# Optimization experiments

Measured on AMD Instinct MI355X. Metric: run time of the kernel, lower is better.

## Reference

```python
import jax, jax.numpy as jnp
import numpy as np

N_IN = 4096      # input features
N_NPB = 64       # neurons (inputs) per branch column
N_B = 64         # branches
N_NEXT_H = 256   # next hidden width
COLS = N_B * N_NEXT_H
BATCH = 128


def setup_inputs() -> dict:
    key = jax.random.key(0)
    k1, k2, k3 = jax.random.split(key, 3)
    x = jax.random.normal(k1, (BATCH, N_IN), dtype=jnp.float32)
    # torch kaiming_normal_ on (n_npb, cols): fan_in = cols, gain = sqrt(2)
    std = np.sqrt(2.0 / COLS).astype(np.float32)
    w = jax.random.normal(k2, (N_NPB, COLS), dtype=jnp.float32) * std
    # random per-column input indices (the module's all_branch_indices)
    idx = jax.random.randint(k3, (N_NPB, COLS), 0, N_IN, dtype=jnp.int32)
    return {"x": x, "w": w, "idx": idx}


def _last_write_mask(idx):
    # (row, col) targets. keep[k, c] is True iff no k' > k has idx[k', c] == idx[k, c].
    eq = idx[:, None, :] == idx[None, :, :]                    # [K, K, C]
    later = jnp.triu(jnp.ones((N_NPB, N_NPB), bool), 1)        # k' > k
    return ~jnp.any(eq & later[:, :, None], axis=1)            # [K, C]


def reference(x, w, idx):
    keep = _last_write_mask(idx)
    w_eff = jnp.where(keep, w, jnp.zeros((), x.dtype))         # [K, C]
    cols = jnp.broadcast_to(jnp.arange(COLS), (N_NPB, COLS))
    # scatter weights into dense [n_in, cols] (equals torch's clone+index_put)
    dense = jnp.zeros((N_IN, COLS), x.dtype).at[idx, cols].add(w_eff)
    out = x @ dense                                            # [B, COLS]
    return out.reshape(-1, N_B, N_NEXT_H)
```

## Files before the change

kernel.cpp:

```cpp
#include <hip/hip_runtime.h>

#define N_IN   4096
#define N_NPB  64
#define COLS   16384
#define BATCH  128

typedef unsigned int       uint;
typedef unsigned short     ushort;
typedef unsigned long long u64;
typedef __attribute__((ext_vector_type(2))) _Float16 h2;


template <int KBASE>
static __device__ __forceinline__ uint compute_bits(const int* __restrict__ ip) {
  int v[64 - KBASE];
#pragma unroll
  for (int k = 0; k < 64 - KBASE; ++k) v[k] = ip[(KBASE + k) * COLS];
  uint bits = 0;
#pragma unroll
  for (int j = 0; j < 16; ++j) {
    uint m = 0xffffffffu;
#pragma unroll
    for (int kp = j + 1; kp < 64 - KBASE; ++kp)
      m = min(m, (uint)(v[j] ^ v[kp]));
    bits |= (m != 0u) ? (1u << j) : 0u;
  }
  return bits;
}

__global__ __launch_bounds__(256, 4) void prep_kernel(
    const float* __restrict__ x, const int* __restrict__ idx,
    ushort* __restrict__ xTh, ushort* __restrict__ keep16) {
  const int bid = blockIdx.x;
  const int tid = threadIdx.x;
  if (bid < 512) {
    __shared__ float tile[32][33];
    const int i0 = (bid & 127) * 32;
    const int b0 = (bid >> 7) * 32;
    const int tx = tid & 31;
    const int ty = tid >> 5;
#pragma unroll
    for (int j = 0; j < 32; j += 8)
      tile[ty + j][tx] = x[(b0 + ty + j) * N_IN + i0 + tx];
    __syncthreads();
#pragma unroll
    for (int j = 0; j < 32; j += 8)
      xTh[(i0 + ty + j) * BATCH + b0 + tx] =
          __builtin_bit_cast(ushort, (_Float16)tile[tx][ty + j]);
  } else {
    const int kg = __builtin_amdgcn_readfirstlane(tid >> 6);
    const int c  = (bid - 512) * 64 + (tid & 63);
    const int* ip = idx + c;
    uint bits;
    if      (kg == 0) bits = compute_bits<0>(ip);
    else if (kg == 1) bits = compute_bits<16>(ip);
    else if (kg == 2) bits = compute_bits<32>(ip);
    else              bits = compute_bits<48>(ip);
    keep16[c * 4 + kg] = (ushort)bits;
  }
}

__global__ __launch_bounds__(512, 8) void branch_main_kernel(
    const float* __restrict__ w, const int* __restrict__ idx,
    const u64* __restrict__ keep, const ushort* __restrict__ xTh,
    float* __restrict__ out) {
  __shared__ u64   pk[N_NPB][16];
  __shared__ float res[2][16][132];

  const int tid = threadIdx.x;
  const int c0  = blockIdx.x * 16;

  {
    const int cl = tid & 15;
    const int k0 = (tid >> 4) * 2;
    const u64 km = keep[c0 + cl];
#pragma unroll
    for (int p = 0; p < 2; ++p) {
      const int k   = k0 + p;
      const int row = idx[k * COLS + c0 + cl];
      float wv      = w[k * COLS + c0 + cl];
      wv = ((km >> k) & 1ull) ? wv : 0.0f;
      const uint hb = (uint)__builtin_bit_cast(ushort, (_Float16)wv);
      pk[k][cl] = ((u64)((hb << 16) | hb) << 32) | ((u64)((uint)row << 8));
    }
  }
  __syncthreads();

  const int wave  = tid >> 6;
  const int khalf = wave >> 2;
  const int lane  = tid & 63;
  const int g     = lane >> 4;
  const int b8    = lane & 15;
  const int cl    = (wave & 3) * 4 + g;

  const char* xb = (const char*)xTh;
  const uint  bo = (uint)b8 * 16;
  const int   kb = khalf * 32;

  h2 a0 = (h2)0.0f, a1 = (h2)0.0f, a2 = (h2)0.0f, a3 = (h2)0.0f;
#pragma unroll
  for (int kk = 0; kk < 32; ++kk) {
    const u64  e   = pk[kb + kk][cl];
    const uint off = (uint)e + bo;
    const h2   wh  = __builtin_bit_cast(h2, (uint)(e >> 32));
    const uint4 u  = *(const uint4*)(xb + off);
    a0 += __builtin_bit_cast(h2, u.x) * wh;
    a1 += __builtin_bit_cast(h2, u.y) * wh;
    a2 += __builtin_bit_cast(h2, u.z) * wh;
    a3 += __builtin_bit_cast(h2, u.w) * wh;
  }

  {
    float* r = &res[khalf][cl][b8 * 8];
    r[0] = (float)a0.x; r[1] = (float)a0.y;
    r[2] = (float)a1.x; r[3] = (float)a1.y;
    r[4] = (float)a2.x; r[5] = (float)a2.y;
    r[6] = (float)a3.x; r[7] = (float)a3.y;
  }
  __syncthreads();

  for (int e = tid; e < BATCH * 16; e += 512) {
    const int b = e >> 4, cc = e & 15;
    out[b * COLS + c0 + cc] = res[0][cc][b] + res[1][cc][b];
  }
}

extern "C" void kernel_launch(void* const* d_in, const int* in_sizes, int n_in,
                              void* d_out, int out_size, void* d_ws, size_t ws_size,
                              hipStream_t stream) {
  const float* x   = (const float*)d_in[0];
  const float* w   = (const float*)d_in[1];
  const int*   idx = (const int*)d_in[2];
  float* out = (float*)d_out;

  char* ws = (char*)d_ws;
  ushort* xTh    = (ushort*)(ws);
  ushort* keep16 = (ushort*)(ws + (1u << 20));
  u64*    keep   = (u64*)(ws + (1u << 20));

  hipLaunchKernelGGL(prep_kernel, dim3(512 + COLS / 64), dim3(256), 0, stream,
                     x, idx, xTh, keep16);
  hipLaunchKernelGGL(branch_main_kernel, dim3(COLS / 16), dim3(512), 0, stream,
                     w, idx, keep, xTh, out);
}
```

Baseline: 23.81 us.

## Quantize transposed activations to int8 with per-feature scales folded into weights

The prep kernel now quantizes x into an offset-biased uint8 transposed layout, using a per-input-feature absmax scale, instead of storing fp16. The main kernel folds that scale into each weight and accumulates in fp32 from byte-decoded values. It subtracts a 128*sum(w) bias term to undo the offset. This halves the bytes of the gathered activation rows, cutting gather traffic. In exchange it adds per-byte convert/FMA ALU work, a cross-lane shuffle reduction, and int8 quantization error versus the reference.

```diff
diff --git a/kernel.cpp b/kernel.cpp
--- a/kernel.cpp
+++ b/kernel.cpp
@@ -7,8 +7,8 @@
 
 typedef unsigned int       uint;
 typedef unsigned short     ushort;
+typedef unsigned char      uchar;
 typedef unsigned long long u64;
-typedef __attribute__((ext_vector_type(2))) _Float16 h2;
 
 
 template <int KBASE>
@@ -30,26 +30,69 @@
 
 __global__ __launch_bounds__(256, 4) void prep_kernel(
     const float* __restrict__ x, const int* __restrict__ idx,
-    ushort* __restrict__ xTh, ushort* __restrict__ keep16) {
+    uchar* __restrict__ x8, float* __restrict__ scl,
+    ushort* __restrict__ keep16) {
   const int bid = blockIdx.x;
   const int tid = threadIdx.x;
-  if (bid < 512) {
-    __shared__ float tile[32][33];
-    const int i0 = (bid & 127) * 32;
-    const int b0 = (bid >> 7) * 32;
-    const int tx = tid & 31;
-    const int ty = tid >> 5;
-#pragma unroll
-    for (int j = 0; j < 32; j += 8)
-      tile[ty + j][tx] = x[(b0 + ty + j) * N_IN + i0 + tx];
-    __syncthreads();
-#pragma unroll
-    for (int j = 0; j < 32; j += 8)
-      xTh[(i0 + ty + j) * BATCH + b0 + tx] =
-          __builtin_bit_cast(ushort, (_Float16)tile[tx][ty + j]);
+  if (bid < 128) {
+    __shared__ float tile[128][33];
+    __shared__ float pmax[8][32];
+    __shared__ float sinv[32];
+    __shared__ uint  qrow[32][32];
+
+    const int i0 = bid * 32;
+    const int f  = tid & 31;
+    const int g  = tid >> 5;
+
+#pragma unroll
+    for (int p = 0; p < 16; ++p) {
+      const int b = p * 8 + g;
+      tile[b][f] = x[b * N_IN + i0 + f];
+    }
+    __syncthreads();
+
+    {
+      float m = 0.0f;
+      const int b0 = g * 16;
+#pragma unroll
+      for (int j = 0; j < 16; ++j) m = fmaxf(m, fabsf(tile[b0 + j][f]));
+      pmax[g][f] = m;
+    }
+    __syncthreads();
+    if (tid < 32) {
+      float m = pmax[0][tid];
+#pragma unroll
+      for (int p = 1; p < 8; ++p) m = fmaxf(m, pmax[p][tid]);
+      m = fmaxf(m, 1e-30f);
+      scl[i0 + tid]  = m * (1.0f / 127.0f);
+      sinv[tid] = 127.0f / m;
+    }
+    __syncthreads();
+
+    {
+      const float iv = sinv[f];
+#pragma unroll
+      for (int p = 0; p < 4; ++p) {
+        const int bq = g + p * 8;
+        uint pk4 = 0;
+#pragma unroll
+        for (int j = 0; j < 4; ++j) {
+          float q = rintf(tile[bq * 4 + j][f] * iv);
+          q = fminf(fmaxf(q, -127.0f), 127.0f);
+          pk4 |= ((uint)(q + 128.0f)) << (8 * j);
+        }
+        qrow[f][bq] = pk4;
+      }
+    }
+    __syncthreads();
+
+    for (int e = tid; e < 32 * 32; e += 256) {
+      const int ff = e >> 5, d = e & 31;
+      ((uint*)x8)[(i0 + ff) * 32 + d] = qrow[ff][d];
+    }
   } else {
     const int kg = __builtin_amdgcn_readfirstlane(tid >> 6);
-    const int c  = (bid - 512) * 64 + (tid & 63);
+    const int c  = (bid - 128) * 64 + (tid & 63);
     const int* ip = idx + c;
     uint bits;
     if      (kg == 0) bits = compute_bits<0>(ip);
@@ -62,8 +105,8 @@
 
 __global__ __launch_bounds__(512, 8) void branch_main_kernel(
     const float* __restrict__ w, const int* __restrict__ idx,
-    const u64* __restrict__ keep, const ushort* __restrict__ xTh,
-    float* __restrict__ out) {
+    const u64* __restrict__ keep, const uchar* __restrict__ x8,
+    const float* __restrict__ scl, float* __restrict__ out) {
   __shared__ u64   pk[N_NPB][16];
   __shared__ float res[2][16][132];
 
@@ -79,9 +122,9 @@
       const int k   = k0 + p;
       const int row = idx[k * COLS + c0 + cl];
       float wv      = w[k * COLS + c0 + cl];
-      wv = ((km >> k) & 1ull) ? wv : 0.0f;
-      const uint hb = (uint)__builtin_bit_cast(ushort, (_Float16)wv);
-      pk[k][cl] = ((u64)((hb << 16) | hb) << 32) | ((u64)((uint)row << 8));
+      wv = ((km >> k) & 1ull) ? wv * scl[row] : 0.0f;
+      pk[k][cl] = ((u64)__builtin_bit_cast(uint, wv) << 32) |
+                  ((u64)((uint)row << 7));
     }
   }
   __syncthreads();
@@ -89,39 +132,63 @@
   const int wave  = tid >> 6;
   const int khalf = wave >> 2;
   const int lane  = tid & 63;
-  const int g     = lane >> 4;
-  const int b8    = lane & 15;
-  const int cl    = (wave & 3) * 4 + g;
-
-  const char* xb = (const char*)xTh;
-  const uint  bo = (uint)b8 * 16;
-  const int   kb = khalf * 32;
-
-  h2 a0 = (h2)0.0f, a1 = (h2)0.0f, a2 = (h2)0.0f, a3 = (h2)0.0f;
-#pragma unroll
-  for (int kk = 0; kk < 32; ++kk) {
-    const u64  e   = pk[kb + kk][cl];
+  const int ksub  = lane >> 5;
+  const int cslot = (lane >> 3) & 3;
+  const int bl    = lane & 7;
+  const int cl    = (wave & 3) * 4 + cslot;
+  const int kb    = khalf * 32;
+
+  const char* xb = (const char*)x8;
+  const uint  bo = (uint)bl * 16;
+
+  float acc[16];
+#pragma unroll
+  for (int j = 0; j < 16; ++j) acc[j] = 0.0f;
+  float wsum = 0.0f;
+
+#pragma unroll
+  for (int kk = 0; kk < 32; kk += 2) {
+    const u64  e   = pk[kb + kk + ksub][cl];
     const uint off = (uint)e + bo;
-    const h2   wh  = __builtin_bit_cast(h2, (uint)(e >> 32));
+    const float wv = __builtin_bit_cast(float, (uint)(e >> 32));
     const uint4 u  = *(const uint4*)(xb + off);
-    a0 += __builtin_bit_cast(h2, u.x) * wh;
-    a1 += __builtin_bit_cast(h2, u.y) * wh;
-    a2 += __builtin_bit_cast(h2, u.z) * wh;
-    a3 += __builtin_bit_cast(h2, u.w) * wh;
-  }
-
-  {
-    float* r = &res[khalf][cl][b8 * 8];
-    r[0] = (float)a0.x; r[1] = (float)a0.y;
-    r[2] = (float)a1.x; r[3] = (float)a1.y;
-    r[4] = (float)a2.x; r[5] = (float)a2.y;
-    r[6] = (float)a3.x; r[7] = (float)a3.y;
+    wsum += wv;
+#define DEC(word, sh) ((float)((word >> sh) & 0xffu))
+    acc[0]  = fmaf(wv, DEC(u.x, 0),  acc[0]);
+    acc[1]  = fmaf(wv, DEC(u.x, 8),  acc[1]);
+    acc[2]  = fmaf(wv, DEC(u.x, 16), acc[2]);
+    acc[3]  = fmaf(wv, DEC(u.x, 24), acc[3]);
+    acc[4]  = fmaf(wv, DEC(u.y, 0),  acc[4]);
+    acc[5]  = fmaf(wv, DEC(u.y, 8),  acc[5]);
+    acc[6]  = fmaf(wv, DEC(u.y, 16), acc[6]);
+    acc[7]  = fmaf(wv, DEC(u.y, 24), acc[7]);
+    acc[8]  = fmaf(wv, DEC(u.z, 0),  acc[8]);
+    acc[9]  = fmaf(wv, DEC(u.z, 8),  acc[9]);
+    acc[10] = fmaf(wv, DEC(u.z, 16), acc[10]);
+    acc[11] = fmaf(wv, DEC(u.z, 24), acc[11]);
+    acc[12] = fmaf(wv, DEC(u.w, 0),  acc[12]);
+    acc[13] = fmaf(wv, DEC(u.w, 8),  acc[13]);
+    acc[14] = fmaf(wv, DEC(u.w, 16), acc[14]);
+    acc[15] = fmaf(wv, DEC(u.w, 24), acc[15]);
+#undef DEC
+  }
+
+#pragma unroll
+  for (int j = 0; j < 16; ++j) acc[j] += __shfl_xor(acc[j], 32);
+  wsum += __shfl_xor(wsum, 32);
+
+  if (lane < 32) {
+    float* r = &res[khalf][cl][bl * 16];
+#pragma unroll
+    for (int j = 0; j < 16; ++j) r[j] = acc[j];
+    if (bl == 0) res[khalf][cl][128] = wsum;
   }
   __syncthreads();
 
   for (int e = tid; e < BATCH * 16; e += 512) {
     const int b = e >> 4, cc = e & 15;
-    out[b * COLS + c0 + cc] = res[0][cc][b] + res[1][cc][b];
+    const float bias = 128.0f * (res[0][cc][128] + res[1][cc][128]);
+    out[b * COLS + c0 + cc] = res[0][cc][b] + res[1][cc][b] - bias;
   }
 }
 
@@ -134,12 +201,13 @@
   float* out = (float*)d_out;
 
   char* ws = (char*)d_ws;
-  ushort* xTh    = (ushort*)(ws);
+  uchar*  x8     = (uchar*)(ws);
+  float*  scl    = (float*)(ws + (512u << 10));
   ushort* keep16 = (ushort*)(ws + (1u << 20));
   u64*    keep   = (u64*)(ws + (1u << 20));
 
-  hipLaunchKernelGGL(prep_kernel, dim3(512 + COLS / 64), dim3(256), 0, stream,
-                     x, idx, xTh, keep16);
+  hipLaunchKernelGGL(prep_kernel, dim3(128 + COLS / 64), dim3(256), 0, stream,
+                     x, idx, x8, scl, keep16);
   hipLaunchKernelGGL(branch_main_kernel, dim3(COLS / 16), dim3(512), 0, stream,
-                     w, idx, keep, xTh, out);
-}
+                     w, idx, keep, x8, scl, out);
+}
```

After: 45.76 us. +92.2%, slower.
